# Optimization experiments

Hardware: AMD Instinct MI355X
Metric: run time of the kernel (lower is better)

## Reference

```python
import jax, jax.numpy as jnp
import numpy as np

B, K, N, E, T = 4096, 64, 100000, 128, 3


def setup_inputs() -> dict:
    key = jax.random.key(0)
    ks = jax.random.split(key, 16)
    f = lambda i, shape: jax.random.normal(ks[i], shape, dtype=jnp.float32) * 0.05
    return dict(
        nodes=jax.random.randint(ks[0], (B,), 0, N),
        neigh_idx=jax.random.randint(ks[1], (T, B, K), 0, N),
        node_emb=f(2, (N, E)),
        node_prof=f(3, (N, E)),
        neigh_emb=f(4, (T, N, E)),
        neigh_prof=f(5, (T, N, E)),
        W_f=f(6, (2 * E, E)), b_f=jnp.zeros((E,), jnp.float32),
        Wa1=f(7, (2 * E, E)), ba1=jnp.zeros((E,), jnp.float32),
        Wa2=f(8, (E, E)), ba2=jnp.zeros((E,), jnp.float32),
        Wa3=f(9, (E, 1)), ba3=jnp.zeros((1,), jnp.float32),
        W1=f(10, (E, E)), b1=jnp.zeros((E,), jnp.float32),
        W2=f(11, (E, E)), b2=jnp.zeros((E,), jnp.float32),
        Wc=f(12, (2 * E, E)), bc=jnp.zeros((E,), jnp.float32),
        Wt=f(13, (T * E, T)),
    )


def reference(nodes, neigh_idx, node_emb, node_prof, neigh_emb, neigh_prof,
              W_f, b_f, Wa1, ba1, Wa2, ba2, Wa3, ba3,
              W1, b1, W2, b2, Wc, bc, Wt):
    # fusion(emb, profile) = relu(Linear(concat(emb, profile)))
    fuse = lambda e, p: jax.nn.relu(jnp.concatenate([e, p], -1) @ W_f + b_f)

    nodes_fusion = fuse(node_emb[nodes], node_prof[nodes])            # [B,E]

    per_type = []
    for t in range(T):                                                 # small fixed loop over types
        idx = neigh_idx[t]                                             # [B,K]
        nf = fuse(neigh_emb[t][idx], neigh_prof[t][idx])               # [B,K,E]
        # attention MLP over (neighbor, node) pairs -> softmax over K neighbors
        x = jnp.concatenate(
            [nf, jnp.broadcast_to(nodes_fusion[:, None, :], nf.shape)], -1)  # [B,K,2E]
        h = jax.nn.relu(x @ Wa1 + ba1)
        h = jax.nn.relu(h @ Wa2 + ba2)
        att = jax.nn.softmax((h @ Wa3 + ba3).squeeze(-1), axis=1)      # [B,K]
        agg = jnp.einsum('bke,bk->be', nf, att)                        # weighted neighbor sum
        per_type.append(jax.nn.relu(agg @ W1 + b1))                    # linear_1 + relu

    type_agg = jnp.concatenate(per_type, axis=1)                       # [B,T*E]
    att_t = jax.nn.softmax(type_agg @ Wt, axis=1)                      # [B,T]
    final = jnp.einsum('bte,bt->be', type_agg.reshape(B, T, E), att_t)
    final = jax.nn.relu(final @ W2 + b2)                               # linear_2 + relu
    out = jax.nn.relu(jnp.concatenate([nodes_fusion, final], 1) @ Wc + bc)
    return out, att_t[:, :, None]
```

## Files before the change

### kernel.cpp

```cpp
#include <hip/hip_runtime.h>
#include <hip/hip_bf16.h>

#define B_ 4096
#define K_ 64
#define N_ 100000
#define E_ 128
#define T_ 3

typedef __bf16 bf16x8 __attribute__((ext_vector_type(8)));
typedef float  f32x4  __attribute__((ext_vector_type(4)));

static __device__ __forceinline__ bf16x8 cvt8r(f32x4 u, f32x4 v) {
    bf16x8 o;
    o[0] = (__bf16)u[0]; o[1] = (__bf16)u[1]; o[2] = (__bf16)u[2]; o[3] = (__bf16)u[3];
    o[4] = (__bf16)v[0]; o[5] = (__bf16)v[1]; o[6] = (__bf16)v[2]; o[7] = (__bf16)v[3];
    return o;
}

typedef const __attribute__((address_space(1))) void GAS;
typedef __attribute__((address_space(3))) void LAS;
static __device__ __forceinline__ void gload16(const void* g, void* l) {
    __builtin_amdgcn_global_load_lds((GAS*)g, (LAS*)l, 16, 0, 0);
}

#define MFMA16(a, b, c) __builtin_amdgcn_mfma_f32_16x16x32_bf16((a), (b), (c), 0, 0, 0)

__global__ __launch_bounds__(256)
void k_prep(const float* __restrict__ W_f, const float* __restrict__ Wa1,
            const float* __restrict__ Wa2, const float* __restrict__ W1,
            __bf16* __restrict__ WtF, __bf16* __restrict__ Wa1t,
            __bf16* __restrict__ Wa2t, __bf16* __restrict__ W1t) {
    const int n = blockIdx.x;
    const int k = threadIdx.x;
    if (blockIdx.y == 0) {
        WtF[n * 256 + k] = (__bf16)W_f[k * 128 + n];
    } else if (blockIdx.y == 1) {
        if (k < 128) Wa1t[n * 128 + k] = (__bf16)Wa1[k * 128 + n];
    } else if (blockIdx.y == 2) {
        if (k < 128) Wa2t[n * 128 + k] = (__bf16)Wa2[k * 128 + n];
    } else {
        if (k < 128) W1t[n * 128 + k] = (__bf16)W1[k * 128 + n];
    }
}

__global__ __launch_bounds__(128)
void k_node_fusion(const int* __restrict__ nodes,
                   const float* __restrict__ node_emb,
                   const float* __restrict__ node_prof,
                   const float* __restrict__ W_f, const float* __restrict__ b_f,
                   __bf16* __restrict__ nodes_fusion) {
    __shared__ float x[256];
    const int b = blockIdx.x;
    const int e = threadIdx.x;
    const int nd = nodes[b];
    x[e]       = node_emb[(size_t)nd * E_ + e];
    x[128 + e] = node_prof[(size_t)nd * E_ + e];
    __syncthreads();
    float acc = b_f[e];
#pragma unroll 8
    for (int i = 0; i < 256; ++i) acc = fmaf(x[i], W_f[i * E_ + e], acc);
    nodes_fusion[(size_t)b * E_ + e] = (__bf16)fmaxf(acc, 0.f);
}

__global__ __launch_bounds__(128)
void k_node_pre(const __bf16* __restrict__ nodes_fusion,
                const float* __restrict__ Wa1, const float* __restrict__ ba1,
                __bf16* __restrict__ node_pre) {
    __shared__ float x[128];
    const int b = blockIdx.x;
    const int c = threadIdx.x;
    x[c] = (float)nodes_fusion[(size_t)b * E_ + c];
    __syncthreads();
    float acc = ba1[c];
#pragma unroll 8
    for (int i = 0; i < 128; ++i) acc = fmaf(x[i], Wa1[(128 + i) * E_ + c], acc);
    node_pre[(size_t)b * E_ + c] = (__bf16)acc;
}

#define NF_GRID 1024
#define NF_TPT (N_ / 16)
#define NF_NJOB (NF_TPT * T_)

__global__ __launch_bounds__(256, 4)
void k_nf(const float* __restrict__ neigh_emb,
          const float* __restrict__ neigh_prof,
          const __bf16* __restrict__ WtF, const float* __restrict__ b_f,
          __bf16* __restrict__ NFt) {
    __shared__ __align__(16) float  Xf[2][16 * 256];
    __shared__ __align__(16) __bf16 NFl[16 * 128];

    const int tid  = threadIdx.x;
    const int wid  = tid >> 6, lane = tid & 63;
    const int lr   = lane & 15, lk = lane >> 4;

    bf16x8 wf[16];
#pragma unroll
    for (int ks = 0; ks < 8; ++ks)
#pragma unroll
        for (int n = 0; n < 2; ++n)
            wf[ks * 2 + n] = *(const bf16x8*)&WtF[
                (size_t)(wid * 32 + n * 16 + lr) * 256 + ks * 32 + lk * 8];
    const float bb0 = b_f[wid * 32 + lr];
    const float bb1 = b_f[wid * 32 + 16 + lr];

    auto stage = [&](int j, int buf) {
        const int t    = j / NF_TPT;
        const int base = (j - t * NF_TPT) * 16;
        const float* embT  = neigh_emb  + (size_t)t * N_ * E_;
        const float* profT = neigh_prof + (size_t)t * N_ * E_;
#pragma unroll
        for (int i = 0; i < 4; ++i) {
            const int r  = wid * 4 + i;
            const int id = base + r;
            const int g  = lane ^ (r & 15);
            const float* src = (g < 32)
                ? embT  + (size_t)id * E_ + g * 4
                : profT + (size_t)id * E_ + (g - 32) * 4;
            gload16(src, (char*)&Xf[buf][0] + r * 1024);
        }
    };

    int job = blockIdx.x;
    stage(job, 0);
    int cur = 0;
    bool first = true;

    for (; job < NF_NJOB; job += NF_GRID) {
        const int tc    = job / NF_TPT;
        const int basec = (job - tc * NF_TPT) * 16;

        if (first) { asm volatile("s_waitcnt vmcnt(0)" ::: "memory"); first = false; }
        else       { asm volatile("s_waitcnt vmcnt(1)" ::: "memory"); }
        __builtin_amdgcn_s_barrier();
        __builtin_amdgcn_sched_barrier(0);

        const int nxt = job + NF_GRID;
        if (nxt < NF_NJOB) stage(nxt, cur ^ 1);

        const float* X = &Xf[cur][0];

        {
            f32x4 acc1[2] = {};
#pragma unroll
            for (int ks = 0; ks < 8; ++ks) {
                const int g0 = ks * 8 + lk * 2;
                const f32x4 u0 = *(const f32x4*)&X[lr * 256 + ((g0 ^ lr) << 2)];
                const f32x4 v0 = *(const f32x4*)&X[lr * 256 + (((g0 + 1) ^ lr) << 2)];
                const bf16x8 a0 = cvt8r(u0, v0);
                acc1[0] = MFMA16(a0, wf[ks * 2 + 0], acc1[0]);
                acc1[1] = MFMA16(a0, wf[ks * 2 + 1], acc1[1]);
            }
#pragma unroll
            for (int n = 0; n < 2; ++n) {
                const int c = wid * 32 + n * 16 + lr;
                const float bb = n ? bb1 : bb0;
                const int q = c >> 3, eo = c & 7;
#pragma unroll
                for (int j = 0; j < 4; ++j) {
                    const int rN = lk * 4 + j;
                    NFl[rN * 128 + ((q ^ rN) << 3) + eo] =
                        (__bf16)fmaxf(acc1[n][j] + bb, 0.f);
                }
            }
        }
        asm volatile("s_waitcnt lgkmcnt(0)" ::: "memory");
        __builtin_amdgcn_s_barrier();
        __builtin_amdgcn_sched_barrier(0);

        {
            const int rr = tid >> 4, qq = tid & 15;
            const int p = qq ^ (rr & 15);
            __bf16* outp = NFt + ((size_t)tc * N_ + basec + rr) * E_ + qq * 8;
            *(bf16x8*)outp = *(const bf16x8*)&NFl[rr * 128 + (p << 3)];
        }
        cur ^= 1;
    }
}

#define ATT_GRID 512
#define ATT_JPB 24

__global__ __launch_bounds__(256, 2)
void k_att(const int* __restrict__ neigh_idx,
           const __bf16* __restrict__ NFt,
           const __bf16* __restrict__ Wa1t,
           const __bf16* __restrict__ Wa2t,
           const float* __restrict__ ba2,
           const float* __restrict__ Wa3, const float* __restrict__ ba3,
           const __bf16* __restrict__ node_pre,
           __bf16* __restrict__ aggB) {
    __shared__ __align__(16) __bf16 Nb[3][64 * 128];
    __shared__ __align__(16) __bf16 H1l[64 * 128];
    __shared__ int    idxL[ATT_JPB * 64];
    __shared__ __bf16 npreL[ATT_JPB * 128];
    __shared__ float  scp[4 * 64];

    float* red4 = (float*)H1l;

    const int tid = threadIdx.x;
    const int wid = tid >> 6, lane = tid & 63;
    const int lr = lane & 15, lk = lane >> 4;
    const int job0 = blockIdx.x * ATT_JPB;

    bf16x8 wa1r[8], wa2r[8];
#pragma unroll
    for (int ks = 0; ks < 4; ++ks)
#pragma unroll
        for (int n = 0; n < 2; ++n) {
            wa1r[ks * 2 + n] = *(const bf16x8*)&Wa1t[
                (size_t)(wid * 32 + n * 16 + lr) * 128 + ks * 32 + lk * 8];
            wa2r[ks * 2 + n] = *(const bf16x8*)&Wa2t[
                (size_t)(wid * 32 + n * 16 + lr) * 128 + ks * 32 + lk * 8];
        }
    float ba2r[2], wa3r[2];
#pragma unroll
    for (int n = 0; n < 2; ++n) {
        ba2r[n] = ba2[wid * 32 + n * 16 + lr];
        wa3r[n] = Wa3[wid * 32 + n * 16 + lr];
    }
    const float ba3v = ba3[0];

#pragma unroll
    for (int i = tid; i < ATT_JPB * 64; i += 256)
        idxL[i] = neigh_idx[(size_t)job0 * K_ + i];
#pragma unroll
    for (int i = tid; i < ATT_JPB * 128; i += 256) {
        const int jj = i >> 7, c = i & 127;
        const int b = (job0 + jj) % B_;
        npreL[i] = node_pre[(size_t)b * E_ + c];
    }
    __syncthreads();

    auto stage = [&](int jj, int buf) {
        const int t = (job0 + jj) / B_;
        const __bf16* tab = NFt + (size_t)t * N_ * E_;
#pragma unroll
        for (int i = 0; i < 4; ++i) {
            const int rowblock = wid * 16 + i * 4;
            const int rsub = i * 4 + (lane >> 4);
            const int q = (lane & 15) ^ rsub;
            const int id = idxL[jj * 64 + wid * 16 + rsub];
            gload16(tab + (size_t)id * E_ + q * 8,
                    (char*)&Nb[buf][0] + rowblock * 256);
        }
    };

    stage(0, 0);
    stage(1, 1);

    for (int it = 0; it < ATT_JPB; ++it) {
        if (it == 0)                 { asm volatile("s_waitcnt vmcnt(4)" ::: "memory"); }
        else if (it >= ATT_JPB - 2)  { asm volatile("s_waitcnt vmcnt(0)" ::: "memory"); }
        else                         { asm volatile("s_waitcnt vmcnt(5)" ::: "memory"); }
        __builtin_amdgcn_s_barrier();
        __builtin_amdgcn_sched_barrier(0);

        if (it + 2 < ATT_JPB) stage(it + 2, (it + 2) % 3);

        const __bf16* NbC = &Nb[it % 3][0];

        {
            f32x4 acc2[4][2] = {};
#pragma unroll
            for (int ks = 0; ks < 4; ++ks) {
                const int q = ks * 4 + lk;
                bf16x8 a[4];
#pragma unroll
                for (int mi = 0; mi < 4; ++mi)
                    a[mi] = *(const bf16x8*)&NbC[(mi * 16 + lr) * 128 + ((q ^ lr) << 3)];
#pragma unroll
                for (int n = 0; n < 2; ++n)
#pragma unroll
                    for (int mi = 0; mi < 4; ++mi)
                        acc2[mi][n] = MFMA16(a[mi], wa1r[ks * 2 + n], acc2[mi][n]);
            }
#pragma unroll
            for (int n = 0; n < 2; ++n) {
                const int col = wid * 32 + n * 16 + lr;
                const float pp = (float)npreL[it * 128 + col];
                const int q = col >> 3, eo = col & 7;
#pragma unroll
                for (int mi = 0; mi < 4; ++mi)
#pragma unroll
                    for (int j = 0; j < 4; ++j) {
                        const int row = mi * 16 + lk * 4 + j;
                        H1l[row * 128 + ((q ^ (row & 15)) << 3) + eo] =
                            (__bf16)fmaxf(acc2[mi][n][j] + pp, 0.f);
                    }
            }
        }
        asm volatile("s_waitcnt lgkmcnt(0)" ::: "memory");
        __builtin_amdgcn_s_barrier();
        __builtin_amdgcn_sched_barrier(0);

        {
            f32x4 acc3[4][2] = {};
#pragma unroll
            for (int ks = 0; ks < 4; ++ks) {
                const int q = ks * 4 + lk;
                bf16x8 a[4];
#pragma unroll
                for (int mi = 0; mi < 4; ++mi)
                    a[mi] = *(const bf16x8*)&H1l[(mi * 16 + lr) * 128 + ((q ^ lr) << 3)];
#pragma unroll
                for (int n = 0; n < 2; ++n)
#pragma unroll
                    for (int mi = 0; mi < 4; ++mi)
                        acc3[mi][n] = MFMA16(a[mi], wa2r[ks * 2 + n], acc3[mi][n]);
            }
#pragma unroll
            for (int mi = 0; mi < 4; ++mi)
#pragma unroll
                for (int j = 0; j < 4; ++j) {
                    float v = fmaxf(acc3[mi][0][j] + ba2r[0], 0.f) * wa3r[0]
                            + fmaxf(acc3[mi][1][j] + ba2r[1], 0.f) * wa3r[1];
                    v += __shfl_xor(v, 1);
                    v += __shfl_xor(v, 2);
                    v += __shfl_xor(v, 4);
                    v += __shfl_xor(v, 8);
                    if (lr == 0)
                        scp[wid * 64 + mi * 16 + lk * 4 + j] = v;
                }
        }
        asm volatile("s_waitcnt lgkmcnt(0)" ::: "memory");
        __builtin_amdgcn_s_barrier();
        __builtin_amdgcn_sched_barrier(0);

        float att;
        {
            const float v = scp[lane] + scp[64 + lane] + scp[128 + lane]
                          + scp[192 + lane] + ba3v;
            float m = v;
#pragma unroll
            for (int o = 32; o > 0; o >>= 1) m = fmaxf(m, __shfl_xor(m, o));
            const float pe = __expf(v - m);
            float s = pe;
#pragma unroll
            for (int o = 32; o > 0; o >>= 1) s += __shfl_xor(s, o);
            att = pe / s;
        }

        {
            float p0 = 0.f, p1 = 0.f;
            const int q0 = lane >> 3, eo = lane & 7;
            const int q1 = (lane + 64) >> 3;
#pragma unroll
            for (int i = 0; i < 16; ++i) {
                const int row = wid * 16 + i;
                const float av = __shfl(att, row);
                p0 = fmaf(av, (float)NbC[row * 128 + ((q0 ^ (row & 15)) << 3) + eo], p0);
                p1 = fmaf(av, (float)NbC[row * 128 + ((q1 ^ (row & 15)) << 3) + eo], p1);
            }
            red4[wid * 128 + lane] = p0;
            red4[wid * 128 + 64 + lane] = p1;
        }
        asm volatile("s_waitcnt lgkmcnt(0)" ::: "memory");
        __builtin_amdgcn_s_barrier();
        __builtin_amdgcn_sched_barrier(0);

        if (lane < 32) {
            const int e = wid * 32 + lane;
            const float s = red4[e] + red4[128 + e] + red4[256 + e] + red4[384 + e];
            const int job = job0 + it;
            const int bcur = job % B_, tcur = job / B_;
            aggB[((size_t)bcur * T_ + tcur) * E_ + e] = (__bf16)s;
        }
    }
}

__global__ __launch_bounds__(256)
void k_w1(const __bf16* __restrict__ aggB, const __bf16* __restrict__ W1t,
          const float* __restrict__ b1, __bf16* __restrict__ type_agg) {
    const int tid  = threadIdx.x;
    const int wid  = tid >> 6;
    const int lane = tid & 63;
    const int lr   = lane & 15;
    const int lk   = lane >> 4;
    const int rbase = blockIdx.x * 64 + wid * 16;

    f32x4 acc[8] = {};
#pragma unroll
    for (int ks = 0; ks < 4; ++ks) {
        const bf16x8 a = *(const bf16x8*)&aggB[(size_t)(rbase + lr) * 128 + ks * 32 + lk * 8];
        const __bf16* wb = W1t + (size_t)lr * 128 + ks * 32 + lk * 8;
#pragma unroll
        for (int n = 0; n < 8; ++n) {
            const bf16x8 w = *(const bf16x8*)(wb + (size_t)n * 16 * 128);
            acc[n] = MFMA16(a, w, acc[n]);
        }
    }
#pragma unroll
    for (int n = 0; n < 8; ++n) {
        const int col = n * 16 + lr;
        const float bb = b1[col];
#pragma unroll
        for (int j = 0; j < 4; ++j) {
            const int row = rbase + lk * 4 + j;
            type_agg[(size_t)row * 128 + col] = (__bf16)fmaxf(acc[n][j] + bb, 0.f);
        }
    }
}

__global__ __launch_bounds__(128)
void k_final(const __bf16* __restrict__ type_agg,
             const __bf16* __restrict__ nodes_fusion,
             const float* __restrict__ Wt,
             const float* __restrict__ W2, const float* __restrict__ b2,
             const float* __restrict__ Wc, const float* __restrict__ bc,
             float* __restrict__ out, float* __restrict__ att_out) {
    __shared__ float ta[384];
    __shared__ float nfu[128];
    __shared__ float fin[128];
    __shared__ float hb[128];
    __shared__ float att[3];
    __shared__ float red[3][128];

    const int b = blockIdx.x;
    const int e = threadIdx.x;

    const float v0 = (float)type_agg[(size_t)b * 384 + e];
    const float v1 = (float)type_agg[(size_t)b * 384 + 128 + e];
    const float v2 = (float)type_agg[(size_t)b * 384 + 256 + e];
    ta[e] = v0; ta[128 + e] = v1; ta[256 + e] = v2;
    nfu[e] = (float)nodes_fusion[(size_t)b * E_ + e];

    float p0, p1, p2;
    {
        const float* w0 = Wt + (size_t)e * 3;
        const float* w1 = Wt + (size_t)(128 + e) * 3;
        const float* w2 = Wt + (size_t)(256 + e) * 3;
        p0 = v0 * w0[0] + v1 * w1[0] + v2 * w2[0];
        p1 = v0 * w0[1] + v1 * w1[1] + v2 * w2[1];
        p2 = v0 * w0[2] + v1 * w1[2] + v2 * w2[2];
    }
    red[0][e] = p0; red[1][e] = p1; red[2][e] = p2;
    __syncthreads();

    if (e < 3) {
        float s = 0.f;
        for (int i = 0; i < 128; ++i) s += red[e][i];
        red[e][0] = s;
    }
    __syncthreads();
    if (e == 0) {
        const float s0 = red[0][0], s1 = red[1][0], s2 = red[2][0];
        const float m  = fmaxf(s0, fmaxf(s1, s2));
        const float e0 = __expf(s0 - m), e1 = __expf(s1 - m), e2 = __expf(s2 - m);
        const float inv = 1.f / (e0 + e1 + e2);
        att[0] = e0 * inv; att[1] = e1 * inv; att[2] = e2 * inv;
    }
    __syncthreads();

    fin[e] = att[0] * ta[e] + att[1] * ta[128 + e] + att[2] * ta[256 + e];
    __syncthreads();

    float acc = b2[e];
#pragma unroll 8
    for (int i = 0; i < 128; ++i) acc = fmaf(fin[i], W2[i * E_ + e], acc);
    hb[e] = fmaxf(acc, 0.f);
    __syncthreads();

    float acc2 = bc[e];
#pragma unroll 8
    for (int i = 0; i < 128; ++i) acc2 = fmaf(nfu[i], Wc[i * E_ + e], acc2);
#pragma unroll 8
    for (int i = 0; i < 128; ++i) acc2 = fmaf(hb[i], Wc[(128 + i) * E_ + e], acc2);
    out[(size_t)b * E_ + e] = fmaxf(acc2, 0.f);

    if (e < 3) att_out[(size_t)b * 3 + e] = att[e];
}

extern "C" void kernel_launch(void* const* d_in, const int* in_sizes, int n_in,
                              void* d_out, int out_size, void* d_ws, size_t ws_size,
                              hipStream_t stream) {
    const int*   nodes      = (const int*)d_in[0];
    const int*   neigh_idx  = (const int*)d_in[1];
    const float* node_emb   = (const float*)d_in[2];
    const float* node_prof  = (const float*)d_in[3];
    const float* neigh_emb  = (const float*)d_in[4];
    const float* neigh_prof = (const float*)d_in[5];
    const float* W_f = (const float*)d_in[6];  const float* b_f = (const float*)d_in[7];
    const float* Wa1 = (const float*)d_in[8];  const float* ba1 = (const float*)d_in[9];
    const float* Wa2 = (const float*)d_in[10]; const float* ba2 = (const float*)d_in[11];
    const float* Wa3 = (const float*)d_in[12]; const float* ba3 = (const float*)d_in[13];
    const float* W1  = (const float*)d_in[14]; const float* b1  = (const float*)d_in[15];
    const float* W2  = (const float*)d_in[16]; const float* b2  = (const float*)d_in[17];
    const float* Wc  = (const float*)d_in[18]; const float* bc  = (const float*)d_in[19];
    const float* Wt  = (const float*)d_in[20];

    float* out     = (float*)d_out;
    float* att_out = out + (size_t)B_ * E_;

    char* ws = (char*)d_ws;
    __bf16* nodes_fusion = (__bf16*)(ws);
    __bf16* node_pre     = (__bf16*)(ws + (1u << 20));
    __bf16* type_agg     = (__bf16*)(ws + (3u << 20));
    __bf16* aggB         = (__bf16*)(ws + (6u << 20));
    __bf16* WtF          = (__bf16*)(ws + (9u << 20));
    __bf16* Wa1t         = (__bf16*)(ws + (9u << 20) + 65536);
    __bf16* Wa2t         = (__bf16*)(ws + (9u << 20) + 98304);
    __bf16* W1t          = (__bf16*)(ws + (9u << 20) + 131072);
    __bf16* NFt          = (__bf16*)(ws + (16u << 20));

    k_prep<<<dim3(128, 4), 256, 0, stream>>>(W_f, Wa1, Wa2, W1, WtF, Wa1t, Wa2t, W1t);
    k_node_fusion<<<B_, 128, 0, stream>>>(nodes, node_emb, node_prof, W_f, b_f,
                                          nodes_fusion);
    k_node_pre<<<B_, 128, 0, stream>>>(nodes_fusion, Wa1, ba1, node_pre);
    k_nf<<<NF_GRID, 256, 0, stream>>>(neigh_emb, neigh_prof, WtF, b_f, NFt);
    k_att<<<ATT_GRID, 256, 0, stream>>>(neigh_idx, NFt, Wa1t, Wa2t, ba2,
                                        Wa3, ba3, node_pre, aggB);
    k_w1<<<(B_ * T_) / 64, 256, 0, stream>>>(aggB, W1t, b1, type_agg);
    k_final<<<B_, 128, 0, stream>>>(type_agg, nodes_fusion, Wt, W2, b2, Wc, bc,
                                    out, att_out);
}
```

Measured before the change: 301.5 us.

## Precompute neighbor Wa1 projection per table row in k_nf, simplify k_att

```diff
diff --git a/kernel.cpp b/kernel.cpp
--- a/kernel.cpp
+++ b/kernel.cpp
@@ -77,15 +77,16 @@
     node_pre[(size_t)b * E_ + c] = (__bf16)acc;
 }
 
-#define NF_GRID 1024
+#define NF_GRID 768
 #define NF_TPT (N_ / 16)
 #define NF_NJOB (NF_TPT * T_)
 
-__global__ __launch_bounds__(256, 4)
+__global__ __launch_bounds__(256, 3)
 void k_nf(const float* __restrict__ neigh_emb,
           const float* __restrict__ neigh_prof,
           const __bf16* __restrict__ WtF, const float* __restrict__ b_f,
-          __bf16* __restrict__ NFt) {
+          const __bf16* __restrict__ Wa1t,
+          __bf16* __restrict__ NFt, __bf16* __restrict__ Gt) {
     __shared__ __align__(16) float  Xf[2][16 * 256];
     __shared__ __align__(16) __bf16 NFl[16 * 128];
 
@@ -100,6 +101,13 @@
         for (int n = 0; n < 2; ++n)
             wf[ks * 2 + n] = *(const bf16x8*)&WtF[
                 (size_t)(wid * 32 + n * 16 + lr) * 256 + ks * 32 + lk * 8];
+    bf16x8 wa1r[8];
+#pragma unroll
+    for (int ks = 0; ks < 4; ++ks)
+#pragma unroll
+        for (int n = 0; n < 2; ++n)
+            wa1r[ks * 2 + n] = *(const bf16x8*)&Wa1t[
+                (size_t)(wid * 32 + n * 16 + lr) * 128 + ks * 32 + lk * 8];
     const float bb0 = b_f[wid * 32 + lr];
     const float bb1 = b_f[wid * 32 + 16 + lr];
 
@@ -125,12 +133,15 @@
     int cur = 0;
     bool first = true;
 
+    const int rr = tid >> 4, qq = tid & 15;
+    const int pp = qq ^ rr;
+
     for (; job < NF_NJOB; job += NF_GRID) {
         const int tc    = job / NF_TPT;
         const int basec = (job - tc * NF_TPT) * 16;
 
         if (first) { asm volatile("s_waitcnt vmcnt(0)" ::: "memory"); first = false; }
-        else       { asm volatile("s_waitcnt vmcnt(1)" ::: "memory"); }
+        else       { asm volatile("s_waitcnt vmcnt(2)" ::: "memory"); }
         __builtin_amdgcn_s_barrier();
         __builtin_amdgcn_sched_barrier(0);
 
@@ -168,168 +179,162 @@
         __builtin_amdgcn_sched_barrier(0);
 
         {
-            const int rr = tid >> 4, qq = tid & 15;
-            const int p = qq ^ (rr & 15);
             __bf16* outp = NFt + ((size_t)tc * N_ + basec + rr) * E_ + qq * 8;
-            *(bf16x8*)outp = *(const bf16x8*)&NFl[rr * 128 + (p << 3)];
+            *(bf16x8*)outp = *(const bf16x8*)&NFl[rr * 128 + (pp << 3)];
+        }
+
+        {
+            f32x4 g[2] = {};
+#pragma unroll
+            for (int ks = 0; ks < 4; ++ks) {
+                const int q = ks * 4 + lk;
+                const bf16x8 a = *(const bf16x8*)&NFl[lr * 128 + ((q ^ lr) << 3)];
+                g[0] = MFMA16(a, wa1r[ks * 2 + 0], g[0]);
+                g[1] = MFMA16(a, wa1r[ks * 2 + 1], g[1]);
+            }
+            __bf16* Gl = (__bf16*)&Xf[cur][0];
+#pragma unroll
+            for (int n = 0; n < 2; ++n) {
+                const int c = wid * 32 + n * 16 + lr;
+                const int q = c >> 3, eo = c & 7;
+#pragma unroll
+                for (int j = 0; j < 4; ++j) {
+                    const int rN = lk * 4 + j;
+                    Gl[rN * 128 + ((q ^ rN) << 3) + eo] = (__bf16)g[n][j];
+                }
+            }
+        }
+        asm volatile("s_waitcnt lgkmcnt(0)" ::: "memory");
+        __builtin_amdgcn_s_barrier();
+        __builtin_amdgcn_sched_barrier(0);
+
+        {
+            const __bf16* Gl = (const __bf16*)&Xf[cur][0];
+            __bf16* outp = Gt + ((size_t)tc * N_ + basec + rr) * E_ + qq * 8;
+            *(bf16x8*)outp = *(const bf16x8*)&Gl[rr * 128 + (pp << 3)];
         }
         cur ^= 1;
     }
 }
 
-#define ATT_GRID 512
-#define ATT_JPB 24
-
-__global__ __launch_bounds__(256, 2)
+#define ATT_JPB 4
+#define ATT_GRID ((B_ * T_) / ATT_JPB)
+
+__global__ __launch_bounds__(256, 3)
 void k_att(const int* __restrict__ neigh_idx,
            const __bf16* __restrict__ NFt,
-           const __bf16* __restrict__ Wa1t,
+           const __bf16* __restrict__ Gt,
            const __bf16* __restrict__ Wa2t,
            const float* __restrict__ ba2,
            const float* __restrict__ Wa3, const float* __restrict__ ba3,
            const __bf16* __restrict__ node_pre,
            __bf16* __restrict__ aggB) {
-    __shared__ __align__(16) __bf16 Nb[3][64 * 128];
-    __shared__ __align__(16) __bf16 H1l[64 * 128];
+    __shared__ __align__(16) __bf16 Gb[2][64 * 128];
+    __shared__ __align__(16) __bf16 Nb[64 * 128];
     __shared__ int    idxL[ATT_JPB * 64];
     __shared__ __bf16 npreL[ATT_JPB * 128];
-    __shared__ float  scp[4 * 64];
-
-    float* red4 = (float*)H1l;
+    __shared__ float  scp[128];
+    __shared__ float  red4[512];
 
     const int tid = threadIdx.x;
     const int wid = tid >> 6, lane = tid & 63;
     const int lr = lane & 15, lk = lane >> 4;
     const int job0 = blockIdx.x * ATT_JPB;
-
-    bf16x8 wa1r[8], wa2r[8];
-#pragma unroll
-    for (int ks = 0; ks < 4; ++ks)
-#pragma unroll
-        for (int n = 0; n < 2; ++n) {
-            wa1r[ks * 2 + n] = *(const bf16x8*)&Wa1t[
-                (size_t)(wid * 32 + n * 16 + lr) * 128 + ks * 32 + lk * 8];
-            wa2r[ks * 2 + n] = *(const bf16x8*)&Wa2t[
-                (size_t)(wid * 32 + n * 16 + lr) * 128 + ks * 32 + lk * 8];
-        }
-    float ba2r[2], wa3r[2];
-#pragma unroll
-    for (int n = 0; n < 2; ++n) {
-        ba2r[n] = ba2[wid * 32 + n * 16 + lr];
-        wa3r[n] = Wa3[wid * 32 + n * 16 + lr];
+    const int t    = job0 / B_;
+    const int b0   = job0 % B_;
+
+    const __bf16* NFtab = NFt + (size_t)t * N_ * E_;
+    const __bf16* Gtab  = Gt  + (size_t)t * N_ * E_;
+
+    const int mp = wid >> 1, h = wid & 1;
+    bf16x8 wa2r[4][4];
+    float ba2r[4], wa3r[4];
+#pragma unroll
+    for (int n = 0; n < 4; ++n) {
+        const int col = h * 64 + n * 16 + lr;
+#pragma unroll
+        for (int ks = 0; ks < 4; ++ks)
+            wa2r[ks][n] = *(const bf16x8*)&Wa2t[(size_t)col * 128 + ks * 32 + lk * 8];
+        ba2r[n] = ba2[col];
+        wa3r[n] = Wa3[col];
     }
     const float ba3v = ba3[0];
 
-#pragma unroll
-    for (int i = tid; i < ATT_JPB * 64; i += 256)
-        idxL[i] = neigh_idx[(size_t)job0 * K_ + i];
+    idxL[tid] = neigh_idx[(size_t)job0 * K_ + tid];
 #pragma unroll
     for (int i = tid; i < ATT_JPB * 128; i += 256) {
         const int jj = i >> 7, c = i & 127;
-        const int b = (job0 + jj) % B_;
-        npreL[i] = node_pre[(size_t)b * E_ + c];
-    }
-    __syncthreads();
-
-    auto stage = [&](int jj, int buf) {
-        const int t = (job0 + jj) / B_;
-        const __bf16* tab = NFt + (size_t)t * N_ * E_;
+        npreL[i] = node_pre[(size_t)(b0 + jj) * E_ + c];
+    }
+    __syncthreads();
+
+    auto stage = [&](const __bf16* tab, int jj, char* dst) {
 #pragma unroll
         for (int i = 0; i < 4; ++i) {
             const int rowblock = wid * 16 + i * 4;
             const int rsub = i * 4 + (lane >> 4);
             const int q = (lane & 15) ^ rsub;
             const int id = idxL[jj * 64 + wid * 16 + rsub];
-            gload16(tab + (size_t)id * E_ + q * 8,
-                    (char*)&Nb[buf][0] + rowblock * 256);
+            gload16(tab + (size_t)id * E_ + q * 8, dst + rowblock * 256);
         }
     };
 
-    stage(0, 0);
-    stage(1, 1);
+    stage(Gtab, 0, (char*)&Gb[0][0]);
 
     for (int it = 0; it < ATT_JPB; ++it) {
-        if (it == 0)                 { asm volatile("s_waitcnt vmcnt(4)" ::: "memory"); }
-        else if (it >= ATT_JPB - 2)  { asm volatile("s_waitcnt vmcnt(0)" ::: "memory"); }
-        else                         { asm volatile("s_waitcnt vmcnt(5)" ::: "memory"); }
+        if (it == 0) { asm volatile("s_waitcnt vmcnt(0)" ::: "memory"); }
+        else         { asm volatile("s_waitcnt vmcnt(1)" ::: "memory"); }
         __builtin_amdgcn_s_barrier();
         __builtin_amdgcn_sched_barrier(0);
 
-        if (it + 2 < ATT_JPB) stage(it + 2, (it + 2) % 3);
-
-        const __bf16* NbC = &Nb[it % 3][0];
-
-        {
-            f32x4 acc2[4][2] = {};
-#pragma unroll
-            for (int ks = 0; ks < 4; ++ks) {
-                const int q = ks * 4 + lk;
-                bf16x8 a[4];
-#pragma unroll
-                for (int mi = 0; mi < 4; ++mi)
-                    a[mi] = *(const bf16x8*)&NbC[(mi * 16 + lr) * 128 + ((q ^ lr) << 3)];
-#pragma unroll
-                for (int n = 0; n < 2; ++n)
-#pragma unroll
-                    for (int mi = 0; mi < 4; ++mi)
-                        acc2[mi][n] = MFMA16(a[mi], wa1r[ks * 2 + n], acc2[mi][n]);
-            }
-#pragma unroll
-            for (int n = 0; n < 2; ++n) {
-                const int col = wid * 32 + n * 16 + lr;
-                const float pp = (float)npreL[it * 128 + col];
-                const int q = col >> 3, eo = col & 7;
-#pragma unroll
-                for (int mi = 0; mi < 4; ++mi)
-#pragma unroll
-                    for (int j = 0; j < 4; ++j) {
-                        const int row = mi * 16 + lk * 4 + j;
-                        H1l[row * 128 + ((q ^ (row & 15)) << 3) + eo] =
-                            (__bf16)fmaxf(acc2[mi][n][j] + pp, 0.f);
-                    }
-            }
-        }
+        stage(NFtab, it, (char*)&Nb[0]);
+        if (it + 1 < ATT_JPB) stage(Gtab, it + 1, (char*)&Gb[(it + 1) & 1][0]);
+
+        const __bf16* GbC = &Gb[it & 1][0];
+
+        f32x4 acc[2][4] = {};
+#pragma unroll
+        for (int ks = 0; ks < 4; ++ks) {
+            const int q = ks * 4 + lk;
+            const bf16x8 g0 = *(const bf16x8*)&GbC[(32 * mp + lr) * 128 + ((q ^ lr) << 3)];
+            const bf16x8 g1 = *(const bf16x8*)&GbC[(32 * mp + 16 + lr) * 128 + ((q ^ lr) << 3)];
+            const bf16x8 np = *(const bf16x8*)&npreL[it * 128 + q * 8];
+            bf16x8 a0, a1;
+#pragma unroll
+            for (int j = 0; j < 8; ++j) {
+                const float nv = (float)np[j];
+                a0[j] = (__bf16)fmaxf((float)g0[j] + nv, 0.f);
+                a1[j] = (__bf16)fmaxf((float)g1[j] + nv, 0.f);
+            }
+#pragma unroll
+            for (int n = 0; n < 4; ++n) {
+                acc[0][n] = MFMA16(a0, wa2r[ks][n], acc[0][n]);
+                acc[1][n] = MFMA16(a1, wa2r[ks][n], acc[1][n]);
+            }
+        }
+
+#pragma unroll
+        for (int mi = 0; mi < 2; ++mi)
+#pragma unroll
+            for (int j = 0; j < 4; ++j) {
+                float v = 0.f;
+#pragma unroll
+                for (int n = 0; n < 4; ++n)
+                    v += fmaxf(acc[mi][n][j] + ba2r[n], 0.f) * wa3r[n];
+                v += __shfl_xor(v, 1);
+                v += __shfl_xor(v, 2);
+                v += __shfl_xor(v, 4);
+                v += __shfl_xor(v, 8);
+                if (lr == 0)
+                    scp[h * 64 + 32 * mp + mi * 16 + lk * 4 + j] = v;
+            }
         asm volatile("s_waitcnt lgkmcnt(0)" ::: "memory");
         __builtin_amdgcn_s_barrier();
         __builtin_amdgcn_sched_barrier(0);
 
-        {
-            f32x4 acc3[4][2] = {};
-#pragma unroll
-            for (int ks = 0; ks < 4; ++ks) {
-                const int q = ks * 4 + lk;
-                bf16x8 a[4];
-#pragma unroll
-                for (int mi = 0; mi < 4; ++mi)
-                    a[mi] = *(const bf16x8*)&H1l[(mi * 16 + lr) * 128 + ((q ^ lr) << 3)];
-#pragma unroll
-                for (int n = 0; n < 2; ++n)
-#pragma unroll
-                    for (int mi = 0; mi < 4; ++mi)
-                        acc3[mi][n] = MFMA16(a[mi], wa2r[ks * 2 + n], acc3[mi][n]);
-            }
-#pragma unroll
-            for (int mi = 0; mi < 4; ++mi)
-#pragma unroll
-                for (int j = 0; j < 4; ++j) {
-                    float v = fmaxf(acc3[mi][0][j] + ba2r[0], 0.f) * wa3r[0]
-                            + fmaxf(acc3[mi][1][j] + ba2r[1], 0.f) * wa3r[1];
-                    v += __shfl_xor(v, 1);
-                    v += __shfl_xor(v, 2);
-                    v += __shfl_xor(v, 4);
-                    v += __shfl_xor(v, 8);
-                    if (lr == 0)
-                        scp[wid * 64 + mi * 16 + lk * 4 + j] = v;
-                }
-        }
-        asm volatile("s_waitcnt lgkmcnt(0)" ::: "memory");
-        __builtin_amdgcn_s_barrier();
-        __builtin_amdgcn_sched_barrier(0);
-
         float att;
         {
-            const float v = scp[lane] + scp[64 + lane] + scp[128 + lane]
-                          + scp[192 + lane] + ba3v;
+            const float v = scp[lane] + scp[64 + lane] + ba3v;
             float m = v;
 #pragma unroll
             for (int o = 32; o > 0; o >>= 1) m = fmaxf(m, __shfl_xor(m, o));
@@ -339,6 +344,10 @@
             for (int o = 32; o > 0; o >>= 1) s += __shfl_xor(s, o);
             att = pe / s;
         }
+
+        if (it + 1 < ATT_JPB) { asm volatile("s_waitcnt vmcnt(4)" ::: "memory"); }
+        else                  { asm volatile("s_waitcnt vmcnt(0)" ::: "memory"); }
+        __builtin_amdgcn_sched_barrier(0);
 
         {
             float p0 = 0.f, p1 = 0.f;
@@ -348,8 +357,8 @@
             for (int i = 0; i < 16; ++i) {
                 const int row = wid * 16 + i;
                 const float av = __shfl(att, row);
-                p0 = fmaf(av, (float)NbC[row * 128 + ((q0 ^ (row & 15)) << 3) + eo], p0);
-                p1 = fmaf(av, (float)NbC[row * 128 + ((q1 ^ (row & 15)) << 3) + eo], p1);
+                p0 = fmaf(av, (float)Nb[row * 128 + ((q0 ^ (row & 15)) << 3) + eo], p0);
+                p1 = fmaf(av, (float)Nb[row * 128 + ((q1 ^ (row & 15)) << 3) + eo], p1);
             }
             red4[wid * 128 + lane] = p0;
             red4[wid * 128 + 64 + lane] = p1;
@@ -361,9 +370,7 @@
         if (lane < 32) {
             const int e = wid * 32 + lane;
             const float s = red4[e] + red4[128 + e] + red4[256 + e] + red4[384 + e];
-            const int job = job0 + it;
-            const int bcur = job % B_, tcur = job / B_;
-            aggB[((size_t)bcur * T_ + tcur) * E_ + e] = (__bf16)s;
+            aggB[((size_t)(b0 + it) * T_ + t) * E_ + e] = (__bf16)s;
         }
     }
 }
@@ -494,20 +501,22 @@
     char* ws = (char*)d_ws;
     __bf16* nodes_fusion = (__bf16*)(ws);
     __bf16* node_pre     = (__bf16*)(ws + (1u << 20));
-    __bf16* type_agg     = (__bf16*)(ws + (3u << 20));
-    __bf16* aggB         = (__bf16*)(ws + (6u << 20));
-    __bf16* WtF          = (__bf16*)(ws + (9u << 20));
-    __bf16* Wa1t         = (__bf16*)(ws + (9u << 20) + 65536);
-    __bf16* Wa2t         = (__bf16*)(ws + (9u << 20) + 98304);
-    __bf16* W1t          = (__bf16*)(ws + (9u << 20) + 131072);
-    __bf16* NFt          = (__bf16*)(ws + (16u << 20));
+    __bf16* type_agg     = (__bf16*)(ws + (2u << 20));
+    __bf16* aggB         = (__bf16*)(ws + (5u << 20));
+    __bf16* WtF          = (__bf16*)(ws + (8u << 20));
+    __bf16* Wa1t         = (__bf16*)(ws + (8u << 20) + 65536);
+    __bf16* Wa2t         = (__bf16*)(ws + (8u << 20) + 98304);
+    __bf16* W1t          = (__bf16*)(ws + (8u << 20) + 131072);
+    __bf16* NFt          = (__bf16*)(ws + (9u << 20));
+    __bf16* Gt           = (__bf16*)(ws + (83u << 20));
 
     k_prep<<<dim3(128, 4), 256, 0, stream>>>(W_f, Wa1, Wa2, W1, WtF, Wa1t, Wa2t, W1t);
     k_node_fusion<<<B_, 128, 0, stream>>>(nodes, node_emb, node_prof, W_f, b_f,
                                           nodes_fusion);
     k_node_pre<<<B_, 128, 0, stream>>>(nodes_fusion, Wa1, ba1, node_pre);
-    k_nf<<<NF_GRID, 256, 0, stream>>>(neigh_emb, neigh_prof, WtF, b_f, NFt);
-    k_att<<<ATT_GRID, 256, 0, stream>>>(neigh_idx, NFt, Wa1t, Wa2t, ba2,
+    k_nf<<<NF_GRID, 256, 0, stream>>>(neigh_emb, neigh_prof, WtF, b_f, Wa1t,
+                                      NFt, Gt);
+    k_att<<<ATT_GRID, 256, 0, stream>>>(neigh_idx, NFt, Gt, Wa2t, ba2,
                                         Wa3, ba3, node_pre, aggB);
     k_w1<<<(B_ * T_) / 64, 256, 0, stream>>>(aggB, W1t, b1, type_agg);
     k_final<<<B_, 128, 0, stream>>>(type_agg, nodes_fusion, Wt, W2, b2, Wc, bc,
```

After: 328.1 us. 8.8% more time.
